# Kernel optimization log

Measured on AMD Instinct MI355X. Metric: run time of the kernel, lower is better.

## Reference

```python
import jax, jax.numpy as jnp
import numpy as np

N = 100000      # nodes
E = 1600000     # edges (avg degree 16)
G = 1000        # graphs in batch
F_IN = 128      # num_features
C = 10          # num_classes
EPS = 1e-5


def setup_inputs() -> dict:
    key = jax.random.key(0)
    ks = jax.random.split(key, 12)
    w = lambda k, shape: jax.random.normal(k, shape, jnp.float32) * 0.05
    return {
        'x': jax.random.normal(ks[0], (N, F_IN), jnp.float32),
        'edge_index': jax.random.randint(ks[1], (2, E), 0, N, jnp.int32),
        'edge_weights': jax.random.randint(ks[2], (E,), 0, 2, jnp.int32),
        'batch': jnp.sort(jax.random.randint(ks[3], (N,), 0, G, jnp.int32)),
        'num_graphs': G,
        # initial MLP: Linear(128,32)+BN+ReLU, Linear(32,32)+BN+ReLU
        'W1': w(ks[4], (F_IN, 32)), 'b1': jnp.zeros(32), 'g1': jnp.ones(32), 'bt1': jnp.zeros(32),
        'W2': w(ks[5], (32, 32)), 'b2': jnp.zeros(32), 'g2': jnp.ones(32), 'bt2': jnp.zeros(32),
        'Wl0': w(ks[6], (32, C)), 'bl0': jnp.zeros(C),   # initial_linear
        'Wg1': w(ks[7], (32, 64)), 'bg1': jnp.zeros(64),  # GCNConv 1
        'Wl1': w(ks[8], (64, C)), 'bl1': jnp.zeros(C),
        'Wg2': w(ks[9], (64, 64)), 'bg2': jnp.zeros(64),  # GCNConv 2
        'Wl2': w(ks[10], (64, C)), 'bl2': jnp.zeros(C),
    }


def _bn(h, gamma, beta):
    # BatchNorm1d in training mode: biased batch statistics over nodes
    mu = h.mean(0)
    var = ((h - mu) ** 2).mean(0)
    return gamma * (h - mu) * jax.lax.rsqrt(var + EPS) + beta


def _gcn(h_in, row, col, w, W, b):
    # PyG GCNConv with self-loops: D^{-1/2}(A+I)D^{-1/2} X W + b,
    # edges with mask weight 0 contribute nothing (incl. to degree).
    n = h_in.shape[0]
    h = h_in @ W
    deg = jax.ops.segment_sum(w, col, num_segments=n) + 1.0  # +1 self-loop
    dinv = jax.lax.rsqrt(deg)
    norm = w * dinv[row] * dinv[col]                  # [E]
    agg = jax.ops.segment_sum(h[row] * norm[:, None], col, num_segments=n)
    agg = agg + h * (dinv * dinv)[:, None]            # self-loop term
    return agg + b


def _pool_max(h, batch, num_graphs):
    # torch_scatter scatter_max readout; empty segments -> 0
    p = jax.ops.segment_max(h, batch, num_segments=num_graphs)
    return jnp.where(jnp.isfinite(p), p, 0.0)


def reference(x, edge_index, edge_weights, batch, num_graphs,
              W1, b1, g1, bt1, W2, b2, g2, bt2, Wl0, bl0,
              Wg1, bg1, Wl1, bl1, Wg2, bg2, Wl2, bl2):
    row, col = edge_index[0], edge_index[1]
    w = (edge_weights == 1).astype(x.dtype)  # boolean edge mask as 0/1 weight
    # initial MLP (dropout treated as identity for deterministic reference)
    h = jax.nn.relu(_bn(x @ W1 + b1, g1, bt1))
    h = jax.nn.relu(_bn(h @ W2 + b2, g2, bt2))
    out = _pool_max(h @ Wl0 + bl0, batch, num_graphs)
    # layer 1
    h = _gcn(h, row, col, w, Wg1, bg1)
    out = out + _pool_max(h, batch, num_graphs) @ Wl1 + bl1
    # layer 2
    h = _gcn(h, row, col, w, Wg2, bg2)
    out = out + _pool_max(h, batch, num_graphs) @ Wl2 + bl2
    return out
```

## Files before the change

### kernel.cpp

```cpp
#include <hip/hip_runtime.h>

#define NN 100000
#define EE 1600000
#define GG 1000
#define BN_EPS 1e-5f
#define NB1 391

__device__ __forceinline__ unsigned encf(float f){
  unsigned u = __float_as_uint(f);
  return (u & 0x80000000u) ? ~u : (u | 0x80000000u);
}
__device__ __forceinline__ float dec0(unsigned e){
  unsigned u = (e & 0x80000000u) ? (e & 0x7fffffffu) : ~e;
  float f = __uint_as_float(u);
  return isfinite(f) ? f : 0.0f;
}
__device__ __forceinline__ unsigned short f2bf(float f){
  unsigned u = __float_as_uint(f);
  u += 0x7FFFu + ((u >> 16) & 1u);
  return (unsigned short)(u >> 16);
}
__device__ __forceinline__ float bf2f(unsigned short s){
  return __uint_as_float(((unsigned)s) << 16);
}

__global__ void k_count(const int* __restrict__ ei, const int* __restrict__ ew,
                        int* __restrict__ cnt){
  int e = blockIdx.x*256 + threadIdx.x;
  if (e < EE && ew[e] == 1) atomicAdd(&cnt[ei[EE + e]], 1);
}

__global__ __launch_bounds__(256) void k_scan1(const int* __restrict__ cnt,
    int* __restrict__ loc, int* __restrict__ bsum){
  __shared__ int sm[256];
  const int i = blockIdx.x*256 + threadIdx.x;
  const int v = (i < NN) ? cnt[i] : 0;
  sm[threadIdx.x] = v;
  __syncthreads();
  for (int off = 1; off < 256; off <<= 1){
    int t = (threadIdx.x >= off) ? sm[threadIdx.x - off] : 0;
    __syncthreads();
    sm[threadIdx.x] += t;
    __syncthreads();
  }
  if (i < NN) loc[i] = sm[threadIdx.x] - v;
  if (threadIdx.x == 255) bsum[blockIdx.x] = sm[255];
}

__global__ __launch_bounds__(512) void k_scan2(const int* __restrict__ bsum,
    int* __restrict__ boff){
  __shared__ int sm[512];
  const int t = threadIdx.x;
  const int v = (t < NB1) ? bsum[t] : 0;
  sm[t] = v;
  __syncthreads();
  for (int off = 1; off < 512; off <<= 1){
    int x = (t >= off) ? sm[t - off] : 0;
    __syncthreads();
    sm[t] += x;
    __syncthreads();
  }
  if (t <= NB1) boff[t] = sm[t] - v;
}

__global__ void k_fin(const int* __restrict__ cnt, const int* __restrict__ loc,
                      const int* __restrict__ boff, float* __restrict__ dinv,
                      int* __restrict__ rowstart, int* __restrict__ fill){
  const int i = blockIdx.x*256 + threadIdx.x;
  if (i < NN){
    int rs = loc[i] + boff[i >> 8];
    rowstart[i] = rs; fill[i] = rs;
    dinv[i] = rsqrtf((float)cnt[i] + 1.0f);
  } else if (i == NN){
    rowstart[NN] = boff[NB1];
  }
}

__global__ void k_scatter(const int* __restrict__ ei, const int* __restrict__ ew,
                          int* __restrict__ fill, int* __restrict__ csr){
  int e = blockIdx.x*256 + threadIdx.x;
  if (e < EE && ew[e] == 1){
    int c = ei[EE + e];
    int pos = atomicAdd(&fill[c], 1);
    csr[pos] = ei[e];
  }
}

__global__ __launch_bounds__(256) void k_gemm1(const float* __restrict__ x,
    const float* __restrict__ W1, const float* __restrict__ b1,
    float* __restrict__ Y1, float* __restrict__ stats){
  __shared__ float xs[32*132];
  __shared__ float Ws[128*32];
  __shared__ float red[64];
  const int tid = threadIdx.x;
  for (int j = tid; j < 1024; j += 256) ((float4*)Ws)[j] = ((const float4*)W1)[j];
  const int r = tid >> 3, cg = tid & 7;
  const float4 bv = ((const float4*)b1)[cg];
  float s0=0,s1=0,s2=0,s3=0,q0=0,q1=0,q2=0,q3=0;
  for (int tile = blockIdx.x; tile < 3125; tile += gridDim.x){
    __syncthreads();
    for (int j = tid; j < 1024; j += 256){
      int rr = j >> 5, kk = j & 31;
      *(float4*)&xs[rr*132 + kk*4] = ((const float4*)x)[(size_t)tile*1024 + j];
    }
    __syncthreads();
    float a0=bv.x, a1=bv.y, a2=bv.z, a3=bv.w;
    const float* xr = &xs[r*132];
    const float* wc = &Ws[cg*4];
    #pragma unroll 8
    for (int k = 0; k < 128; k++){
      float xv = xr[k];
      float4 w = *(const float4*)&wc[k*32];
      a0 += xv*w.x; a1 += xv*w.y; a2 += xv*w.z; a3 += xv*w.w;
    }
    float4 o; o.x=a0; o.y=a1; o.z=a2; o.w=a3;
    ((float4*)Y1)[(size_t)(tile*32 + r)*8 + cg] = o;
    s0+=a0; s1+=a1; s2+=a2; s3+=a3;
    q0+=a0*a0; q1+=a1*a1; q2+=a2*a2; q3+=a3*a3;
  }
  __syncthreads();
  if (tid < 64) red[tid] = 0.f;
  __syncthreads();
  atomicAdd(&red[cg*4+0], s0); atomicAdd(&red[cg*4+1], s1);
  atomicAdd(&red[cg*4+2], s2); atomicAdd(&red[cg*4+3], s3);
  atomicAdd(&red[32+cg*4+0], q0); atomicAdd(&red[32+cg*4+1], q1);
  atomicAdd(&red[32+cg*4+2], q2); atomicAdd(&red[32+cg*4+3], q3);
  __syncthreads();
  if (tid < 64) atomicAdd(&stats[tid], red[tid]);
}

__global__ void k_stats(float* __restrict__ stats, const float* __restrict__ gamma,
                        const float* __restrict__ beta, int base){
  int c = threadIdx.x;
  float mean = stats[base + c] * (1.0f/NN);
  float var  = stats[base + 32 + c] * (1.0f/NN) - mean*mean;
  float sc = gamma[c] * rsqrtf(fmaxf(var, 0.0f) + BN_EPS);
  stats[base + 64 + c] = sc;
  stats[base + 96 + c] = beta[c] - mean*sc;
}

__global__ __launch_bounds__(256) void k_mlp2(const float* __restrict__ Y1,
    const float* __restrict__ W2, const float* __restrict__ b2,
    float* __restrict__ stats, float* __restrict__ Y2){
  __shared__ float hs[32*36];
  __shared__ float Ws[32*32];
  __shared__ float red[64];
  const int tid = threadIdx.x;
  ((float4*)Ws)[tid] = ((const float4*)W2)[tid];
  const int r = tid >> 3, cg = tid & 7;
  const float4 bv = ((const float4*)b2)[cg];
  const float4 sc = ((const float4*)(stats + 64))[cg];
  const float4 sh = ((const float4*)(stats + 96))[cg];
  float s0=0,s1=0,s2=0,s3=0,q0=0,q1=0,q2=0,q3=0;
  for (int tile = blockIdx.x; tile < 3125; tile += gridDim.x){
    __syncthreads();
    {
      float4 v = ((const float4*)Y1)[(size_t)tile*256 + tid];
      v.x = fmaxf(fmaf(v.x, sc.x, sh.x), 0.f);
      v.y = fmaxf(fmaf(v.y, sc.y, sh.y), 0.f);
      v.z = fmaxf(fmaf(v.z, sc.z, sh.z), 0.f);
      v.w = fmaxf(fmaf(v.w, sc.w, sh.w), 0.f);
      *(float4*)&hs[r*36 + cg*4] = v;
    }
    __syncthreads();
    float a0=bv.x, a1=bv.y, a2=bv.z, a3=bv.w;
    const float* hr = &hs[r*36];
    const float* wc = &Ws[cg*4];
    #pragma unroll
    for (int k = 0; k < 32; k++){
      float h = hr[k];
      float4 w = *(const float4*)&wc[k*32];
      a0 += h*w.x; a1 += h*w.y; a2 += h*w.z; a3 += h*w.w;
    }
    float4 o; o.x=a0; o.y=a1; o.z=a2; o.w=a3;
    ((float4*)Y2)[(size_t)(tile*32 + r)*8 + cg] = o;
    s0+=a0; s1+=a1; s2+=a2; s3+=a3;
    q0+=a0*a0; q1+=a1*a1; q2+=a2*a2; q3+=a3*a3;
  }
  __syncthreads();
  if (tid < 64) red[tid] = 0.f;
  __syncthreads();
  atomicAdd(&red[cg*4+0], s0); atomicAdd(&red[cg*4+1], s1);
  atomicAdd(&red[cg*4+2], s2); atomicAdd(&red[cg*4+3], s3);
  atomicAdd(&red[32+cg*4+0], q0); atomicAdd(&red[32+cg*4+1], q1);
  atomicAdd(&red[32+cg*4+2], q2); atomicAdd(&red[32+cg*4+3], q3);
  __syncthreads();
  if (tid < 64) atomicAdd(&stats[128 + tid], red[tid]);
}

__global__ __launch_bounds__(256) void k_layer0(const float* __restrict__ Y2,
    const float* __restrict__ stats, const float* __restrict__ Wg1,
    const float* __restrict__ Wl0, const float* __restrict__ bl0,
    const int* __restrict__ batch,
    unsigned short* __restrict__ Hg1, unsigned* __restrict__ Pool0){
  __shared__ float hs[32*36];
  __shared__ float Wg[32*64];
  __shared__ float Wl[320];
  __shared__ float bl[10];
  const int tid = threadIdx.x;
  ((float4*)Wg)[tid]       = ((const float4*)Wg1)[tid];
  ((float4*)Wg)[tid + 256] = ((const float4*)Wg1)[tid + 256];
  for (int j = tid; j < 320; j += 256) Wl[j] = Wl0[j];
  if (tid < 10)  bl[tid] = bl0[tid];
  {
    const int rr = tid >> 3, kk = tid & 7;
    const float4 sc = ((const float4*)(stats + 192))[kk];
    const float4 sh = ((const float4*)(stats + 224))[kk];
    float4 v = ((const float4*)Y2)[(size_t)blockIdx.x*256 + tid];
    v.x = fmaxf(fmaf(v.x, sc.x, sh.x), 0.f);
    v.y = fmaxf(fmaf(v.y, sc.y, sh.y), 0.f);
    v.z = fmaxf(fmaf(v.z, sc.z, sh.z), 0.f);
    v.w = fmaxf(fmaf(v.w, sc.w, sh.w), 0.f);
    *(float4*)&hs[rr*36 + kk*4] = v;
  }
  __syncthreads();
  const int w = tid >> 6, f = tid & 63;
  for (int i = 0; i < 8; i++){
    const int r = w*8 + i;
    const int row = blockIdx.x*32 + r;
    const float* hr = &hs[r*36];
    float acc = 0.f;
    #pragma unroll
    for (int k = 0; k < 32; k++) acc += hr[k]*Wg[k*64 + f];
    Hg1[(size_t)row*64 + f] = f2bf(acc);
    if (f < 10){
      float p = bl[f];
      #pragma unroll
      for (int k = 0; k < 32; k++) p += hr[k]*Wl[k*10 + f];
      atomicMax(&Pool0[batch[row]*10 + f], encf(p));
    }
  }
}

template<bool STORE>
__global__ __launch_bounds__(256) void k_agg(const unsigned short* __restrict__ Hb,
    const float* __restrict__ dinv, const int* __restrict__ rowstart,
    const int* __restrict__ csr, const float* __restrict__ bias,
    const int* __restrict__ batch, float* __restrict__ outp,
    unsigned* __restrict__ Pool){
  __shared__ float sm[4][64];
  __shared__ int sb[4];
  const int w = threadIdx.x >> 6, f = threadIdx.x & 63;
  const int c = blockIdx.x*4 + w;
  const int s = rowstart[c], e = rowstart[c+1];
  float acc = 0.f;
  int j = s;
  for (; j + 3 < e; j += 4){
    const int r0 = csr[j], r1 = csr[j+1], r2 = csr[j+2], r3 = csr[j+3];
    const float d0 = dinv[r0], d1 = dinv[r1], d2 = dinv[r2], d3 = dinv[r3];
    const float h0 = bf2f(Hb[(size_t)r0*64 + f]);
    const float h1 = bf2f(Hb[(size_t)r1*64 + f]);
    const float h2 = bf2f(Hb[(size_t)r2*64 + f]);
    const float h3 = bf2f(Hb[(size_t)r3*64 + f]);
    acc = fmaf(h0, d0, acc); acc = fmaf(h1, d1, acc);
    acc = fmaf(h2, d2, acc); acc = fmaf(h3, d3, acc);
  }
  for (; j < e; j++){
    const int r = csr[j];
    acc = fmaf(bf2f(Hb[(size_t)r*64 + f]), dinv[r], acc);
  }
  const float dc = dinv[c];
  float h = fmaf(acc, dc, bf2f(Hb[(size_t)c*64 + f])*dc*dc) + bias[f];
  if (STORE) outp[(size_t)c*64 + f] = h;
  sm[w][f] = h;
  if (f == 0) sb[w] = batch[c];
  __syncthreads();
  if (w == 0){
    const int b0 = sb[0], b1 = sb[1], b2 = sb[2], b3 = sb[3];
    if (b0 == b3){
      float m = fmaxf(fmaxf(sm[0][f], sm[1][f]), fmaxf(sm[2][f], sm[3][f]));
      atomicMax(&Pool[b0*64 + f], encf(m));
    } else {
      atomicMax(&Pool[b0*64 + f], encf(sm[0][f]));
      atomicMax(&Pool[b1*64 + f], encf(sm[1][f]));
      atomicMax(&Pool[b2*64 + f], encf(sm[2][f]));
      atomicMax(&Pool[b3*64 + f], encf(sm[3][f]));
    }
  }
}

__global__ __launch_bounds__(256) void k_layer1(const float* __restrict__ H2,
    const float* __restrict__ Wg2, unsigned short* __restrict__ Hg2){
  __shared__ float as[32*68];
  __shared__ float Wg[64*64];
  const int tid = threadIdx.x;
  #pragma unroll
  for (int j = 0; j < 4; j++) ((float4*)Wg)[tid + j*256] = ((const float4*)Wg2)[tid + j*256];
  #pragma unroll
  for (int j = 0; j < 2; j++){
    int idx = tid + j*256;
    int rr = idx >> 4, kk = idx & 15;
    *(float4*)&as[rr*68 + kk*4] = ((const float4*)H2)[(size_t)blockIdx.x*512 + idx];
  }
  __syncthreads();
  const int w = tid >> 6, f = tid & 63;
  for (int i = 0; i < 8; i++){
    const int r = w*8 + i;
    const float* ar = &as[r*68];
    float acc = 0.f;
    #pragma unroll
    for (int k = 0; k < 64; k++) acc += ar[k]*Wg[k*64 + f];
    Hg2[(size_t)(blockIdx.x*32 + r)*64 + f] = f2bf(acc);
  }
}

__global__ __launch_bounds__(256) void k_final(const unsigned* __restrict__ P0,
    const unsigned* __restrict__ P1, const unsigned* __restrict__ P2,
    const float* __restrict__ Wl1, const float* __restrict__ bl1,
    const float* __restrict__ Wl2, const float* __restrict__ bl2,
    float* __restrict__ out){
  const int t = blockIdx.x*256 + threadIdx.x;
  const int g = t >> 4, c = t & 15;
  if (g >= GG || c >= 10) return;
  float acc = dec0(P0[g*10 + c]) + bl1[c] + bl2[c];
  for (int f = 0; f < 64; f++){
    acc += dec0(P1[g*64 + f]) * Wl1[f*10 + c];
    acc += dec0(P2[g*64 + f]) * Wl2[f*10 + c];
  }
  out[g*10 + c] = acc;
}

extern "C" void kernel_launch(void* const* d_in, const int* in_sizes, int n_in,
                              void* d_out, int out_size, void* d_ws, size_t ws_size,
                              hipStream_t stream){
  const float* x   = (const float*)d_in[0];
  const int*   ei  = (const int*)d_in[1];
  const int*   ew  = (const int*)d_in[2];
  const int*   bat = (const int*)d_in[3];
  const float* W1  = (const float*)d_in[5],  *b1  = (const float*)d_in[6];
  const float* g1  = (const float*)d_in[7],  *bt1 = (const float*)d_in[8];
  const float* W2  = (const float*)d_in[9],  *b2  = (const float*)d_in[10];
  const float* g2  = (const float*)d_in[11], *bt2 = (const float*)d_in[12];
  const float* Wl0 = (const float*)d_in[13], *bl0 = (const float*)d_in[14];
  const float* Wg1 = (const float*)d_in[15], *bg1 = (const float*)d_in[16];
  const float* Wl1 = (const float*)d_in[17], *bl1 = (const float*)d_in[18];
  const float* Wg2 = (const float*)d_in[19], *bg2 = (const float*)d_in[20];
  const float* Wl2 = (const float*)d_in[21], *bl2 = (const float*)d_in[22];

  float* ws = (float*)d_ws;
  const size_t oCnt   = 0;
  const size_t oStats = NN;
  const size_t oP0    = oStats + 256;
  const size_t oP1    = oP0 + (size_t)GG*10;
  const size_t oP2    = oP1 + (size_t)GG*64;
  const size_t oZEnd  = oP2 + (size_t)GG*64;
  const size_t oDinv  = oZEnd;
  const size_t oLoc   = oDinv + NN;
  const size_t oBsum  = oLoc + NN;
  const size_t oBoff  = oBsum + 512;
  const size_t oRS    = oBoff + 512;
  const size_t oFill  = oRS + NN + 8;
  const size_t oCsr   = oFill + NN;
  const size_t oA     = oCsr + EE;
  const size_t oHgb   = oA + (size_t)NN*64;

  int*   cnt   = (int*)(ws + oCnt);
  float* stats = ws + oStats;
  unsigned* P0 = (unsigned*)(ws + oP0);
  unsigned* P1 = (unsigned*)(ws + oP1);
  unsigned* P2 = (unsigned*)(ws + oP2);
  float* dinv  = ws + oDinv;
  int*   loc   = (int*)(ws + oLoc);
  int*   bsum  = (int*)(ws + oBsum);
  int*   boff  = (int*)(ws + oBoff);
  int*   rs    = (int*)(ws + oRS);
  int*   fill  = (int*)(ws + oFill);
  int*   csr   = (int*)(ws + oCsr);
  float* Y1    = ws + oA;
  float* Y2    = ws + oA + (size_t)NN*32;
  float* H2    = ws + oA;
  unsigned short* Hgb = (unsigned short*)(ws + oHgb);

  (void)hipMemsetAsync(d_ws, 0, oZEnd*sizeof(float), stream);

  k_count  <<<EE/256, 256, 0, stream>>>(ei, ew, cnt);
  k_scan1  <<<NB1, 256, 0, stream>>>(cnt, loc, bsum);
  k_scan2  <<<1, 512, 0, stream>>>(bsum, boff);
  k_fin    <<<NB1, 256, 0, stream>>>(cnt, loc, boff, dinv, rs, fill);
  k_scatter<<<EE/256, 256, 0, stream>>>(ei, ew, fill, csr);

  k_gemm1<<<1536, 256, 0, stream>>>(x, W1, b1, Y1, stats);
  k_stats<<<1, 32, 0, stream>>>(stats, g1, bt1, 0);
  k_mlp2 <<<1536, 256, 0, stream>>>(Y1, W2, b2, stats, Y2);
  k_stats<<<1, 32, 0, stream>>>(stats, g2, bt2, 128);
  k_layer0<<<3125, 256, 0, stream>>>(Y2, stats, Wg1, Wl0, bl0, bat, Hgb, P0);
  k_agg<true> <<<NN/4, 256, 0, stream>>>(Hgb, dinv, rs, csr, bg1, bat, H2, P1);
  k_layer1<<<3125, 256, 0, stream>>>(H2, Wg2, Hgb);
  k_agg<false><<<NN/4, 256, 0, stream>>>(Hgb, dinv, rs, csr, bg2, bat, nullptr, P2);
  k_final<<<(GG*16 + 255)/256, 256, 0, stream>>>(P0, P1, P2, Wl1, bl1, Wl2, bl2, (float*)d_out);
}
```

Baseline: 343.6 us.

## Prescale features by dinv, fuse second GCN GEMM into aggregation, inline BN stats

The GCN features are now pre-multiplied by the source node's dinv when they are produced, so the gather loop no longer loads dinv per edge and only sums bf16 values. The layer-2 linear transform (64x64 GEMM) is fused into the first aggregation kernel, which removes the separate k_layer1 launch and the fp32 H2 round trip through memory. The two tiny k_stats launches are folded into the consuming kernels, which now compute BN scale and shift per block. In exchange, every aggregation block loads a 16KB weight tile into shared memory, which may lower occupancy, and each block recomputes the BN stats redundantly.

```diff
diff --git a/kernel.cpp b/kernel.cpp
--- a/kernel.cpp
+++ b/kernel.cpp
@@ -129,28 +129,27 @@
   if (tid < 64) atomicAdd(&stats[tid], red[tid]);
 }
 
-__global__ void k_stats(float* __restrict__ stats, const float* __restrict__ gamma,
-                        const float* __restrict__ beta, int base){
-  int c = threadIdx.x;
-  float mean = stats[base + c] * (1.0f/NN);
-  float var  = stats[base + 32 + c] * (1.0f/NN) - mean*mean;
-  float sc = gamma[c] * rsqrtf(fmaxf(var, 0.0f) + BN_EPS);
-  stats[base + 64 + c] = sc;
-  stats[base + 96 + c] = beta[c] - mean*sc;
-}
-
 __global__ __launch_bounds__(256) void k_mlp2(const float* __restrict__ Y1,
     const float* __restrict__ W2, const float* __restrict__ b2,
+    const float* __restrict__ g1, const float* __restrict__ bt1,
     float* __restrict__ stats, float* __restrict__ Y2){
   __shared__ float hs[32*36];
   __shared__ float Ws[32*32];
   __shared__ float red[64];
+  __shared__ float scs[32], shs[32];
   const int tid = threadIdx.x;
   ((float4*)Ws)[tid] = ((const float4*)W2)[tid];
+  if (tid < 32){
+    float mean = stats[tid] * (1.0f/NN);
+    float var  = stats[32 + tid] * (1.0f/NN) - mean*mean;
+    float s = g1[tid] * rsqrtf(fmaxf(var, 0.0f) + BN_EPS);
+    scs[tid] = s; shs[tid] = bt1[tid] - mean*s;
+  }
+  __syncthreads();
   const int r = tid >> 3, cg = tid & 7;
   const float4 bv = ((const float4*)b2)[cg];
-  const float4 sc = ((const float4*)(stats + 64))[cg];
-  const float4 sh = ((const float4*)(stats + 96))[cg];
+  const float4 sc = *(const float4*)&scs[cg*4];
+  const float4 sh = *(const float4*)&shs[cg*4];
   float s0=0,s1=0,s2=0,s3=0,q0=0,q1=0,q2=0,q3=0;
   for (int tile = blockIdx.x; tile < 3125; tile += gridDim.x){
     __syncthreads();
@@ -189,23 +188,32 @@
 }
 
 __global__ __launch_bounds__(256) void k_layer0(const float* __restrict__ Y2,
-    const float* __restrict__ stats, const float* __restrict__ Wg1,
+    const float* __restrict__ stats, const float* __restrict__ g2,
+    const float* __restrict__ bt2, const float* __restrict__ Wg1,
     const float* __restrict__ Wl0, const float* __restrict__ bl0,
-    const int* __restrict__ batch,
-    unsigned short* __restrict__ Hg1, unsigned* __restrict__ Pool0){
+    const float* __restrict__ dinv, const int* __restrict__ batch,
+    unsigned short* __restrict__ Hs1, unsigned* __restrict__ Pool0){
   __shared__ float hs[32*36];
   __shared__ float Wg[32*64];
   __shared__ float Wl[320];
   __shared__ float bl[10];
+  __shared__ float scs[32], shs[32];
   const int tid = threadIdx.x;
   ((float4*)Wg)[tid]       = ((const float4*)Wg1)[tid];
   ((float4*)Wg)[tid + 256] = ((const float4*)Wg1)[tid + 256];
   for (int j = tid; j < 320; j += 256) Wl[j] = Wl0[j];
   if (tid < 10)  bl[tid] = bl0[tid];
+  if (tid < 32){
+    float mean = stats[128 + tid] * (1.0f/NN);
+    float var  = stats[160 + tid] * (1.0f/NN) - mean*mean;
+    float s = g2[tid] * rsqrtf(fmaxf(var, 0.0f) + BN_EPS);
+    scs[tid] = s; shs[tid] = bt2[tid] - mean*s;
+  }
+  __syncthreads();
   {
     const int rr = tid >> 3, kk = tid & 7;
-    const float4 sc = ((const float4*)(stats + 192))[kk];
-    const float4 sh = ((const float4*)(stats + 224))[kk];
+    const float4 sc = *(const float4*)&scs[kk*4];
+    const float4 sh = *(const float4*)&shs[kk*4];
     float4 v = ((const float4*)Y2)[(size_t)blockIdx.x*256 + tid];
     v.x = fmaxf(fmaf(v.x, sc.x, sh.x), 0.f);
     v.y = fmaxf(fmaf(v.y, sc.y, sh.y), 0.f);
@@ -222,7 +230,7 @@
     float acc = 0.f;
     #pragma unroll
     for (int k = 0; k < 32; k++) acc += hr[k]*Wg[k*64 + f];
-    Hg1[(size_t)row*64 + f] = f2bf(acc);
+    Hs1[(size_t)row*64 + f] = f2bf(acc * dinv[row]);
     if (f < 10){
       float p = bl[f];
       #pragma unroll
@@ -232,36 +240,36 @@
   }
 }
 
-template<bool STORE>
-__global__ __launch_bounds__(256) void k_agg(const unsigned short* __restrict__ Hb,
+template<bool GEMM>
+__global__ __launch_bounds__(256) void k_agg(const unsigned short* __restrict__ Hs,
     const float* __restrict__ dinv, const int* __restrict__ rowstart,
     const int* __restrict__ csr, const float* __restrict__ bias,
-    const int* __restrict__ batch, float* __restrict__ outp,
-    unsigned* __restrict__ Pool){
+    const int* __restrict__ batch, const float* __restrict__ Wg2,
+    unsigned short* __restrict__ Hs2out, unsigned* __restrict__ Pool){
   __shared__ float sm[4][64];
   __shared__ int sb[4];
-  const int w = threadIdx.x >> 6, f = threadIdx.x & 63;
+  __shared__ float WgL[GEMM ? 64*64 : 4];
+  const int tid = threadIdx.x;
+  if (GEMM){
+    #pragma unroll
+    for (int j = 0; j < 4; j++)
+      ((float4*)WgL)[tid + j*256] = ((const float4*)Wg2)[tid + j*256];
+  }
+  const int w = tid >> 6, f = tid & 63;
   const int c = blockIdx.x*4 + w;
   const int s = rowstart[c], e = rowstart[c+1];
   float acc = 0.f;
   int j = s;
   for (; j + 3 < e; j += 4){
     const int r0 = csr[j], r1 = csr[j+1], r2 = csr[j+2], r3 = csr[j+3];
-    const float d0 = dinv[r0], d1 = dinv[r1], d2 = dinv[r2], d3 = dinv[r3];
-    const float h0 = bf2f(Hb[(size_t)r0*64 + f]);
-    const float h1 = bf2f(Hb[(size_t)r1*64 + f]);
-    const float h2 = bf2f(Hb[(size_t)r2*64 + f]);
-    const float h3 = bf2f(Hb[(size_t)r3*64 + f]);
-    acc = fmaf(h0, d0, acc); acc = fmaf(h1, d1, acc);
-    acc = fmaf(h2, d2, acc); acc = fmaf(h3, d3, acc);
-  }
-  for (; j < e; j++){
-    const int r = csr[j];
-    acc = fmaf(bf2f(Hb[(size_t)r*64 + f]), dinv[r], acc);
-  }
+    acc += bf2f(Hs[(size_t)r0*64 + f]);
+    acc += bf2f(Hs[(size_t)r1*64 + f]);
+    acc += bf2f(Hs[(size_t)r2*64 + f]);
+    acc += bf2f(Hs[(size_t)r3*64 + f]);
+  }
+  for (; j < e; j++) acc += bf2f(Hs[(size_t)csr[j]*64 + f]);
   const float dc = dinv[c];
-  float h = fmaf(acc, dc, bf2f(Hb[(size_t)c*64 + f])*dc*dc) + bias[f];
-  if (STORE) outp[(size_t)c*64 + f] = h;
+  const float h = fmaf(acc + bf2f(Hs[(size_t)c*64 + f]), dc, bias[f]);
   sm[w][f] = h;
   if (f == 0) sb[w] = batch[c];
   __syncthreads();
@@ -277,30 +285,12 @@
       atomicMax(&Pool[b3*64 + f], encf(sm[3][f]));
     }
   }
-}
-
-__global__ __launch_bounds__(256) void k_layer1(const float* __restrict__ H2,
-    const float* __restrict__ Wg2, unsigned short* __restrict__ Hg2){
-  __shared__ float as[32*68];
-  __shared__ float Wg[64*64];
-  const int tid = threadIdx.x;
-  #pragma unroll
-  for (int j = 0; j < 4; j++) ((float4*)Wg)[tid + j*256] = ((const float4*)Wg2)[tid + j*256];
-  #pragma unroll
-  for (int j = 0; j < 2; j++){
-    int idx = tid + j*256;
-    int rr = idx >> 4, kk = idx & 15;
-    *(float4*)&as[rr*68 + kk*4] = ((const float4*)H2)[(size_t)blockIdx.x*512 + idx];
-  }
-  __syncthreads();
-  const int w = tid >> 6, f = tid & 63;
-  for (int i = 0; i < 8; i++){
-    const int r = w*8 + i;
-    const float* ar = &as[r*68];
-    float acc = 0.f;
-    #pragma unroll
-    for (int k = 0; k < 64; k++) acc += ar[k]*Wg[k*64 + f];
-    Hg2[(size_t)(blockIdx.x*32 + r)*64 + f] = f2bf(acc);
+  if (GEMM){
+    float ga = 0.f;
+    const float* hr = sm[w];
+    #pragma unroll 16
+    for (int k = 0; k < 64; k++) ga = fmaf(hr[k], WgL[k*64 + f], ga);
+    Hs2out[(size_t)c*64 + f] = f2bf(ga * dc);
   }
 }
 
@@ -352,7 +342,7 @@
   const size_t oFill  = oRS + NN + 8;
   const size_t oCsr   = oFill + NN;
   const size_t oA     = oCsr + EE;
-  const size_t oHgb   = oA + (size_t)NN*64;
+  const size_t oHs1   = oA + (size_t)NN*64;
 
   int*   cnt   = (int*)(ws + oCnt);
   float* stats = ws + oStats;
@@ -368,8 +358,8 @@
   int*   csr   = (int*)(ws + oCsr);
   float* Y1    = ws + oA;
   float* Y2    = ws + oA + (size_t)NN*32;
-  float* H2    = ws + oA;
-  unsigned short* Hgb = (unsigned short*)(ws + oHgb);
+  unsigned short* Hs2 = (unsigned short*)(ws + oA);
+  unsigned short* Hs1 = (unsigned short*)(ws + oHs1);
 
   (void)hipMemsetAsync(d_ws, 0, oZEnd*sizeof(float), stream);
 
@@ -380,12 +370,9 @@
   k_scatter<<<EE/256, 256, 0, stream>>>(ei, ew, fill, csr);
 
   k_gemm1<<<1536, 256, 0, stream>>>(x, W1, b1, Y1, stats);
-  k_stats<<<1, 32, 0, stream>>>(stats, g1, bt1, 0);
-  k_mlp2 <<<1536, 256, 0, stream>>>(Y1, W2, b2, stats, Y2);
-  k_stats<<<1, 32, 0, stream>>>(stats, g2, bt2, 128);
-  k_layer0<<<3125, 256, 0, stream>>>(Y2, stats, Wg1, Wl0, bl0, bat, Hgb, P0);
-  k_agg<true> <<<NN/4, 256, 0, stream>>>(Hgb, dinv, rs, csr, bg1, bat, H2, P1);
-  k_layer1<<<3125, 256, 0, stream>>>(H2, Wg2, Hgb);
-  k_agg<false><<<NN/4, 256, 0, stream>>>(Hgb, dinv, rs, csr, bg2, bat, nullptr, P2);
+  k_mlp2 <<<1536, 256, 0, stream>>>(Y1, W2, b2, g1, bt1, stats, Y2);
+  k_layer0<<<3125, 256, 0, stream>>>(Y2, stats, g2, bt2, Wg1, Wl0, bl0, dinv, bat, Hs1, P0);
+  k_agg<true> <<<NN/4, 256, 0, stream>>>(Hs1, dinv, rs, csr, bg1, bat, Wg2, Hs2, P1);
+  k_agg<false><<<NN/4, 256, 0, stream>>>(Hs2, dinv, rs, csr, bg2, bat, nullptr, nullptr, P2);
   k_final<<<(GG*16 + 255)/256, 256, 0, stream>>>(P0, P1, P2, Wl1, bl1, Wl2, bl2, (float*)d_out);
 }
```

New measurement: 338.4 us. Within noise of the previous version (-1.5%).
